# Kernel tuning notes

Hardware: AMD Instinct MI355X
Metric: run time of the kernel (lower is better)

The kernel has to match this reference:

```python
import jax, jax.numpy as jnp
import numpy as np

NUM_CLASSES = 10
WEIGHT = tuple([0.1] * NUM_CLASSES)
EXPONENT = 2


def setup_inputs() -> dict:
    key = jax.random.key(0)
    k1, k2, k3 = jax.random.split(key, 3)
    B, Y, X = 64, 512, 512
    outputs = jax.random.normal(k1, (B, Y, X), dtype=jnp.float32)
    # targets hold integer intensity classes 0..9 stored as floats (original does float subtraction)
    targets = jax.random.randint(k2, (B, Y, X), 0, NUM_CLASSES).astype(jnp.float32)
    # observation-station mask: 1 where a station exists, 0 elsewhere
    mask = jax.random.randint(k3, (B, Y, X), 0, 2).astype(jnp.int32)
    return {"outputs": outputs, "targets": targets, "mask": mask}


def reference(outputs, targets, mask):
    # Class id per pixel; invalid (mask==0) pixels routed to dummy segment NUM_CLASSES.
    cls = targets.astype(jnp.int32)
    valid = mask == 1
    ids = jnp.where(valid, cls, NUM_CLASSES).ravel()  # [B*Y*X]

    sqerr = (outputs - targets) ** EXPONENT  # [B,Y,X]
    # One fused scatter-reduce replaces the original triple Python loop over 10 masks.
    per_class_sum = jax.ops.segment_sum(sqerr.ravel(), ids, num_segments=NUM_CLASSES + 1)[:NUM_CLASSES]
    class_n = jax.ops.segment_sum(jnp.ones_like(sqerr).ravel(), ids, num_segments=NUM_CLASSES + 1)[:NUM_CLASSES]

    loss_each = jnp.where(class_n > 0, per_class_sum / jnp.maximum(class_n, 1.0), 0.0)  # [10]
    weight = jnp.asarray(WEIGHT, dtype=outputs.dtype)
    loss = jnp.sum(weight * loss_each)
    return loss, loss_each, class_n
```

## Files before the change

### kernel.cpp

```cpp
#include <hip/hip_runtime.h>

#define NCLS 10
#define ACC_STRIDE 64


__global__ __launch_bounds__(256) void loss_main_kernel(
    const float* __restrict__ outputs,
    const float* __restrict__ targets,
    const int*   __restrict__ mask,
    float* __restrict__ ws,
    int n4)
{
    float sum[NCLS];
    float cnt[NCLS];
#pragma unroll
    for (int c = 0; c < NCLS; ++c) { sum[c] = 0.0f; cnt[c] = 0.0f; }

    const float4* o4 = (const float4*)outputs;
    const float4* t4 = (const float4*)targets;
    const int4*   m4 = (const int4*)mask;

    int tid    = blockIdx.x * blockDim.x + threadIdx.x;
    int stride = gridDim.x * blockDim.x;

    for (int i = tid; i < n4; i += stride) {
        float4 o = o4[i];
        float4 t = t4[i];
        int4   m = m4[i];

        float od[4] = {o.x, o.y, o.z, o.w};
        float td[4] = {t.x, t.y, t.z, t.w};
        int   md[4] = {m.x, m.y, m.z, m.w};

#pragma unroll
        for (int j = 0; j < 4; ++j) {
            float d  = od[j] - td[j];
            float sq = d * d;
            int cls = (md[j] == 1) ? (int)td[j] : NCLS;
#pragma unroll
            for (int c = 0; c < NCLS; ++c) {
                float match = (cls == c) ? 1.0f : 0.0f;
                cnt[c] += match;
                sum[c] = fmaf(match, sq, sum[c]);
            }
        }
    }

#pragma unroll
    for (int c = 0; c < NCLS; ++c) {
#pragma unroll
        for (int off = 32; off > 0; off >>= 1) {
            sum[c] += __shfl_down(sum[c], off, 64);
            cnt[c] += __shfl_down(cnt[c], off, 64);
        }
    }

    __shared__ float ls[4][2 * NCLS];
    int wave = threadIdx.x >> 6;
    int lane = threadIdx.x & 63;
    if (lane == 0) {
#pragma unroll
        for (int c = 0; c < NCLS; ++c) {
            ls[wave][c]        = sum[c];
            ls[wave][NCLS + c] = cnt[c];
        }
    }
    __syncthreads();

    if (threadIdx.x < 2 * NCLS) {
        float v = ls[0][threadIdx.x] + ls[1][threadIdx.x]
                + ls[2][threadIdx.x] + ls[3][threadIdx.x];
        atomicAdd(&ws[threadIdx.x * ACC_STRIDE], v);
    }
}

__global__ __launch_bounds__(64) void loss_final_kernel(
    const float* __restrict__ ws,
    float* __restrict__ out)
{
    int lane = threadIdx.x;
    float le = 0.0f;
    if (lane < NCLS) {
        float s  = ws[lane * ACC_STRIDE];
        float cn = ws[(NCLS + lane) * ACC_STRIDE];
        le = (cn > 0.0f) ? (s / fmaxf(cn, 1.0f)) : 0.0f;
        out[1 + lane]  = le;
        out[11 + lane] = cn;
    }
    float w = 0.1f * le;
#pragma unroll
    for (int off = 32; off > 0; off >>= 1) w += __shfl_down(w, off, 64);
    if (lane == 0) out[0] = w;
}

extern "C" void kernel_launch(void* const* d_in, const int* in_sizes, int n_in,
                              void* d_out, int out_size, void* d_ws, size_t ws_size,
                              hipStream_t stream)
{
    const float* outputs = (const float*)d_in[0];
    const float* targets = (const float*)d_in[1];
    const int*   mask    = (const int*)d_in[2];
    float* out = (float*)d_out;
    float* ws  = (float*)d_ws;

    int n  = in_sizes[0];
    int n4 = n / 4;

    hipMemsetAsync(d_ws, 0, 2 * NCLS * ACC_STRIDE * sizeof(float), stream);

    loss_main_kernel<<<1024, 256, 0, stream>>>(outputs, targets, mask, ws, n4);
    loss_final_kernel<<<1, 64, 0, stream>>>(ws, out);
}
```

Measured before the change: 199.7 us.

## Use wave ballot counts, two loads per iteration, and per-block partials instead of atomics

Per-class counts now come from a wave-wide ballot plus popcount instead of per-thread float accumulation, and class matching compares floats directly. Each thread loads two float4 chunks per iteration to get more memory requests in flight, and the grid doubles to 2048 blocks. Global atomics and the memset are replaced by per-block partial sums that the final kernel reduces with 256 threads. In exchange, every wave now executes ten ballots per element, and the final reduction has to read 2048 partials per class.

```diff
diff --git a/kernel.cpp b/kernel.cpp
--- a/kernel.cpp
+++ b/kernel.cpp
@@ -1,10 +1,11 @@
 #include <hip/hip_runtime.h>
 
 #define NCLS 10
-#define ACC_STRIDE 64
+#define NBLK 2048
+#define TPB  256
 
 
-__global__ __launch_bounds__(256) void loss_main_kernel(
+__global__ __launch_bounds__(TPB) void loss_main_kernel(
     const float* __restrict__ outputs,
     const float* __restrict__ targets,
     const int*   __restrict__ mask,
@@ -12,36 +13,45 @@
     int n4)
 {
     float sum[NCLS];
-    float cnt[NCLS];
 #pragma unroll
-    for (int c = 0; c < NCLS; ++c) { sum[c] = 0.0f; cnt[c] = 0.0f; }
+    for (int c = 0; c < NCLS; ++c) sum[c] = 0.0f;
+    int wcnt[NCLS];
+#pragma unroll
+    for (int c = 0; c < NCLS; ++c) wcnt[c] = 0;
 
     const float4* o4 = (const float4*)outputs;
     const float4* t4 = (const float4*)targets;
     const int4*   m4 = (const int4*)mask;
 
-    int tid    = blockIdx.x * blockDim.x + threadIdx.x;
-    int stride = gridDim.x * blockDim.x;
+    const int tid = blockIdx.x * TPB + threadIdx.x;
+    const int T   = NBLK * TPB;
 
-    for (int i = tid; i < n4; i += stride) {
-        float4 o = o4[i];
-        float4 t = t4[i];
-        int4   m = m4[i];
+    for (int i = tid; i < n4; i += 2 * T) {
+        float4 o0 = o4[i];
+        float4 t0 = t4[i];
+        int4   m0 = m4[i];
+        bool has2 = (i + T) < n4;
+        int i2 = has2 ? (i + T) : i;
+        float4 o1 = o4[i2];
+        float4 t1 = t4[i2];
+        int4   m1 = m4[i2];
 
-        float od[4] = {o.x, o.y, o.z, o.w};
-        float td[4] = {t.x, t.y, t.z, t.w};
-        int   md[4] = {m.x, m.y, m.z, m.w};
+        float od[8] = {o0.x, o0.y, o0.z, o0.w, o1.x, o1.y, o1.z, o1.w};
+        float td[8] = {t0.x, t0.y, t0.z, t0.w, t1.x, t1.y, t1.z, t1.w};
+        int   md[8] = {m0.x, m0.y, m0.z, m0.w, m1.x, m1.y, m1.z, m1.w};
+        int lim = has2 ? 8 : 4;
 
 #pragma unroll
-        for (int j = 0; j < 4; ++j) {
+        for (int j = 0; j < 8; ++j) {
+            if (j >= lim) break;
             float d  = od[j] - td[j];
             float sq = d * d;
-            int cls = (md[j] == 1) ? (int)td[j] : NCLS;
+            float tm = (md[j] == 1) ? td[j] : 10.0f;
 #pragma unroll
             for (int c = 0; c < NCLS; ++c) {
-                float match = (cls == c) ? 1.0f : 0.0f;
-                cnt[c] += match;
-                sum[c] = fmaf(match, sq, sum[c]);
+                bool pred = (tm == (float)c);
+                wcnt[c] += (int)__popcll(__ballot(pred));
+                sum[c]  += pred ? sq : 0.0f;
             }
         }
     }
@@ -49,48 +59,81 @@
 #pragma unroll
     for (int c = 0; c < NCLS; ++c) {
 #pragma unroll
-        for (int off = 32; off > 0; off >>= 1) {
+        for (int off = 32; off > 0; off >>= 1)
             sum[c] += __shfl_down(sum[c], off, 64);
-            cnt[c] += __shfl_down(cnt[c], off, 64);
-        }
     }
 
-    __shared__ float ls[4][2 * NCLS];
+    __shared__ float lsS[4][NCLS];
+    __shared__ float lsC[4][NCLS];
     int wave = threadIdx.x >> 6;
     int lane = threadIdx.x & 63;
     if (lane == 0) {
 #pragma unroll
         for (int c = 0; c < NCLS; ++c) {
-            ls[wave][c]        = sum[c];
-            ls[wave][NCLS + c] = cnt[c];
+            lsS[wave][c] = sum[c];
+            lsC[wave][c] = (float)wcnt[c];
         }
     }
     __syncthreads();
 
     if (threadIdx.x < 2 * NCLS) {
-        float v = ls[0][threadIdx.x] + ls[1][threadIdx.x]
-                + ls[2][threadIdx.x] + ls[3][threadIdx.x];
-        atomicAdd(&ws[threadIdx.x * ACC_STRIDE], v);
+        int c = (threadIdx.x < NCLS) ? threadIdx.x : (threadIdx.x - NCLS);
+        float v;
+        if (threadIdx.x < NCLS)
+            v = lsS[0][c] + lsS[1][c] + lsS[2][c] + lsS[3][c];
+        else
+            v = lsC[0][c] + lsC[1][c] + lsC[2][c] + lsC[3][c];
+        ws[threadIdx.x * NBLK + blockIdx.x] = v;
     }
 }
 
-__global__ __launch_bounds__(64) void loss_final_kernel(
+__global__ __launch_bounds__(TPB) void loss_final_kernel(
     const float* __restrict__ ws,
     float* __restrict__ out)
 {
-    int lane = threadIdx.x;
-    float le = 0.0f;
-    if (lane < NCLS) {
-        float s  = ws[lane * ACC_STRIDE];
-        float cn = ws[(NCLS + lane) * ACC_STRIDE];
-        le = (cn > 0.0f) ? (s / fmaxf(cn, 1.0f)) : 0.0f;
-        out[1 + lane]  = le;
-        out[11 + lane] = cn;
+    float acc[2 * NCLS];
+#pragma unroll
+    for (int k = 0; k < 2 * NCLS; ++k) acc[k] = 0.0f;
+
+    for (int b = threadIdx.x; b < NBLK; b += TPB) {
+#pragma unroll
+        for (int k = 0; k < 2 * NCLS; ++k)
+            acc[k] += ws[k * NBLK + b];
     }
-    float w = 0.1f * le;
+
 #pragma unroll
-    for (int off = 32; off > 0; off >>= 1) w += __shfl_down(w, off, 64);
-    if (lane == 0) out[0] = w;
+    for (int k = 0; k < 2 * NCLS; ++k) {
+#pragma unroll
+        for (int off = 32; off > 0; off >>= 1)
+            acc[k] += __shfl_down(acc[k], off, 64);
+    }
+
+    __shared__ float ls[4][2 * NCLS];
+    __shared__ float lloss[NCLS];
+    int wave = threadIdx.x >> 6;
+    int lane = threadIdx.x & 63;
+    if (lane == 0) {
+#pragma unroll
+        for (int k = 0; k < 2 * NCLS; ++k) ls[wave][k] = acc[k];
+    }
+    __syncthreads();
+
+    if (threadIdx.x < NCLS) {
+        int c = threadIdx.x;
+        float s  = ls[0][c] + ls[1][c] + ls[2][c] + ls[3][c];
+        float cn = ls[0][NCLS + c] + ls[1][NCLS + c] + ls[2][NCLS + c] + ls[3][NCLS + c];
+        float le = (cn > 0.0f) ? (s / fmaxf(cn, 1.0f)) : 0.0f;
+        out[1 + c]  = le;
+        out[11 + c] = cn;
+        lloss[c] = 0.1f * le;
+    }
+    __syncthreads();
+    if (threadIdx.x == 0) {
+        float w = 0.0f;
+#pragma unroll
+        for (int c = 0; c < NCLS; ++c) w += lloss[c];
+        out[0] = w;
+    }
 }
 
 extern "C" void kernel_launch(void* const* d_in, const int* in_sizes, int n_in,
@@ -106,8 +149,6 @@
     int n  = in_sizes[0];
     int n4 = n / 4;
 
-    hipMemsetAsync(d_ws, 0, 2 * NCLS * ACC_STRIDE * sizeof(float), stream);
-
-    loss_main_kernel<<<1024, 256, 0, stream>>>(outputs, targets, mask, ws, n4);
-    loss_final_kernel<<<1, 64, 0, stream>>>(ws, out);
+    loss_main_kernel<<<NBLK, TPB, 0, stream>>>(outputs, targets, mask, ws, n4);
+    loss_final_kernel<<<1, TPB, 0, stream>>>(ws, out);
 }
```

New measurement: 206.7 us. 1.04x slower.
